# Performance work log

Measured on AMD Instinct MI355X. Metric: run time of the kernel, lower is better.

The kernel has to match this reference:

```python
import jax, jax.numpy as jnp
import numpy as np

N, T = 64, 256
TOTAL_NODES, C_IN = 25, 128          # c = 3200
NUM_SEEDS, C_OUT = 5, 3              # seeds flat dim = 15
NEW_NODES = 20
LIN_IN = TOTAL_NODES * C_IN + NUM_SEEDS * C_OUT  # 3215


def setup_inputs() -> dict:
    key = jax.random.key(0)
    k1, k2, k3 = jax.random.split(key, 3)
    x = jax.random.normal(k1, (N, T, TOTAL_NODES * C_IN), dtype=jnp.float32)
    seeds = jax.random.normal(k2, (N, T, NUM_SEEDS, C_OUT), dtype=jnp.float32)
    # Stacked weights of the `new_nodes` cloned Linear(LIN_IN, C_OUT) layers.
    W = jax.random.normal(k3, (NEW_NODES, C_OUT, LIN_IN), dtype=jnp.float32) * 0.02
    b = jnp.zeros((NEW_NODES, C_OUT), dtype=jnp.float32)
    return {"x": x, "seeds": seeds, "W": W, "b": b}


def reference(x, seeds, W, b):
    n, t, _ = x.shape
    mix = jnp.concatenate([x, seeds.reshape(n, t, -1)], axis=2)  # [n,t,LIN_IN]
    # Fuse all cloned small Linears into one batched GEMM, then layout as
    # torch.stack([...], dim=3): output [n, t, c_out, new_nodes].
    out = jnp.einsum('ntc,koc->ntok', mix, W) + b.T  # b.T: [c_out, new_nodes]
    return out
```

## Files before the change

### kernel.cpp

```cpp
#include <hip/hip_runtime.h>


#define NROWS    16384
#define CIN      3200
#define SEED_K   15
#define LIN_IN   3215
#define NCOL     60
#define KB_MAIN  100
#define KB_TOT   101
#define KB_CHUNK 25
#define WB_ELEMS (KB_TOT * 4 * 64 * 8)

typedef __attribute__((ext_vector_type(8))) __bf16 bf16x8;
typedef __attribute__((ext_vector_type(4))) float f32x4;
typedef __attribute__((ext_vector_type(8))) unsigned short ushort8;

__device__ unsigned short Wb_g[WB_ELEMS];

__device__ inline unsigned short f2bf_rne(float f) {
    unsigned int u = __builtin_bit_cast(unsigned int, f);
    u += 0x7fffu + ((u >> 16) & 1u);
    return (unsigned short)(u >> 16);
}

__device__ inline bf16x8 to_bf16x8(f32x4 a0, f32x4 a1) {
    ushort8 u;
    u[0] = f2bf_rne(a0[0]); u[1] = f2bf_rne(a0[1]);
    u[2] = f2bf_rne(a0[2]); u[3] = f2bf_rne(a0[3]);
    u[4] = f2bf_rne(a1[0]); u[5] = f2bf_rne(a1[1]);
    u[6] = f2bf_rne(a1[2]); u[7] = f2bf_rne(a1[3]);
    return __builtin_bit_cast(bf16x8, u);
}

__global__ void prep_B(const float* __restrict__ W) {
    int idx = blockIdx.x * blockDim.x + threadIdx.x;
    if (idx >= WB_ELEMS) return;
    int jj   = idx & 7;
    int lane = (idx >> 3) & 63;
    int nt   = (idx >> 9) & 3;
    int kb   = idx >> 11;
    int k = kb * 32 + (lane >> 4) * 8 + jj;
    int n = nt * 16 + (lane & 15);
    float v = 0.0f;
    if (k < LIN_IN && n < NCOL) {
        int o = n / 20, kn = n % 20;
        v = W[(kn * 3 + o) * LIN_IN + k];
    }
    Wb_g[idx] = f2bf_rne(v);
}

__global__ __launch_bounds__(256, 4) void gen_nodes_gemm(
    const float* __restrict__ x, const float* __restrict__ seeds,
    const float* __restrict__ b, float* __restrict__ out) {
    const int lane = threadIdx.x & 63;
    const int wave = threadIdx.x >> 6;
    const int quad = lane >> 4;
    const int l15  = lane & 15;
    const int row_base = blockIdx.x * 16;
    const int arow = row_base + l15;

    const float* xrow = x + (size_t)arow * CIN + quad * 8;

    f32x4 acc[4];
#pragma unroll
    for (int i = 0; i < 4; ++i) acc[i] = (f32x4){0.f, 0.f, 0.f, 0.f};

    const int kb0 = wave * KB_CHUNK;
    const int kb1 = kb0 + KB_CHUNK;

#pragma unroll 2
    for (int kb = kb0; kb < kb1; ++kb) {
        const f32x4* ap = (const f32x4*)(xrow + kb * 32);
        f32x4 a0 = ap[0];
        f32x4 a1 = ap[1];
        const unsigned short* bb = Wb_g + (size_t)kb * 2048 + lane * 8;
        bf16x8 b0 = *(const bf16x8*)(bb);
        bf16x8 b1 = *(const bf16x8*)(bb + 512);
        bf16x8 b2 = *(const bf16x8*)(bb + 1024);
        bf16x8 b3 = *(const bf16x8*)(bb + 1536);
        bf16x8 af = to_bf16x8(a0, a1);
        acc[0] = __builtin_amdgcn_mfma_f32_16x16x32_bf16(af, b0, acc[0], 0, 0, 0);
        acc[1] = __builtin_amdgcn_mfma_f32_16x16x32_bf16(af, b1, acc[1], 0, 0, 0);
        acc[2] = __builtin_amdgcn_mfma_f32_16x16x32_bf16(af, b2, acc[2], 0, 0, 0);
        acc[3] = __builtin_amdgcn_mfma_f32_16x16x32_bf16(af, b3, acc[3], 0, 0, 0);
    }

    if (wave == 3) {
        const float* srow = seeds + (size_t)arow * SEED_K;
        f32x4 s0 = {0.f, 0.f, 0.f, 0.f}, s1 = {0.f, 0.f, 0.f, 0.f};
#pragma unroll
        for (int j = 0; j < 4; ++j) {
            int c = quad * 8 + j;
            if (c < SEED_K) s0[j] = srow[c];
            if (c + 4 < SEED_K) s1[j] = srow[c + 4];
        }
        bf16x8 af = to_bf16x8(s0, s1);
        const unsigned short* bb = Wb_g + (size_t)KB_MAIN * 2048 + lane * 8;
        bf16x8 b0 = *(const bf16x8*)(bb);
        bf16x8 b1 = *(const bf16x8*)(bb + 512);
        bf16x8 b2 = *(const bf16x8*)(bb + 1024);
        bf16x8 b3 = *(const bf16x8*)(bb + 1536);
        acc[0] = __builtin_amdgcn_mfma_f32_16x16x32_bf16(af, b0, acc[0], 0, 0, 0);
        acc[1] = __builtin_amdgcn_mfma_f32_16x16x32_bf16(af, b1, acc[1], 0, 0, 0);
        acc[2] = __builtin_amdgcn_mfma_f32_16x16x32_bf16(af, b2, acc[2], 0, 0, 0);
        acc[3] = __builtin_amdgcn_mfma_f32_16x16x32_bf16(af, b3, acc[3], 0, 0, 0);
    }

    __shared__ float red[3][16][68];
    if (wave != 0) {
#pragma unroll
        for (int nt = 0; nt < 4; ++nt)
#pragma unroll
            for (int r = 0; r < 4; ++r)
                red[wave - 1][quad * 4 + r][nt * 16 + l15] = acc[nt][r];
    }
    __syncthreads();

    if (wave == 0) {
#pragma unroll
        for (int nt = 0; nt < 4; ++nt) {
            int j = nt * 16 + l15;
            if (j < NCOL) {
                float bias = b[(j % 20) * 3 + (j / 20)];
#pragma unroll
                for (int r = 0; r < 4; ++r) {
                    int m = quad * 4 + r;
                    float v = acc[nt][r] + red[0][m][j] + red[1][m][j]
                            + red[2][m][j] + bias;
                    out[(size_t)(row_base + m) * NCOL + j] = v;
                }
            }
        }
    }
}

extern "C" void kernel_launch(void* const* d_in, const int* in_sizes, int n_in,
                              void* d_out, int out_size, void* d_ws, size_t ws_size,
                              hipStream_t stream) {
    const float* x     = (const float*)d_in[0];
    const float* seeds = (const float*)d_in[1];
    const float* W     = (const float*)d_in[2];
    const float* b     = (const float*)d_in[3];
    float* out = (float*)d_out;
    (void)d_ws; (void)ws_size;

    prep_B<<<(WB_ELEMS + 255) / 256, 256, 0, stream>>>(W);
    gen_nodes_gemm<<<NROWS / 16, 256, 0, stream>>>(x, seeds, b, out);
}
```

Before: 306.8 us.

## Split K across two blocks per row group with prefetch and separate combine kernel

The GEMM is split so that each 16-row group is handled by two blocks, each covering half of K. Within each half the four waves interleave k-blocks with a stride of four, the next A tile is prefetched with nontemporal loads, and occupancy hints are raised. Partial sums go to a workspace and a new combine kernel adds the two halves plus a precomputed bias. The goal is more blocks in flight to hide the latency of the memory-bound x stream, at the cost of an extra kernel launch and a round trip of partials through memory.

```diff
diff --git a/kernel.cpp b/kernel.cpp
--- a/kernel.cpp
+++ b/kernel.cpp
@@ -8,14 +8,15 @@
 #define NCOL     60
 #define KB_MAIN  100
 #define KB_TOT   101
-#define KB_CHUNK 25
 #define WB_ELEMS (KB_TOT * 4 * 64 * 8)
+#define PART_N   (NROWS * NCOL)
 
 typedef __attribute__((ext_vector_type(8))) __bf16 bf16x8;
 typedef __attribute__((ext_vector_type(4))) float f32x4;
 typedef __attribute__((ext_vector_type(8))) unsigned short ushort8;
 
 __device__ unsigned short Wb_g[WB_ELEMS];
+__device__ __align__(16) float bias_g[64];
 
 __device__ inline unsigned short f2bf_rne(float f) {
     unsigned int u = __builtin_bit_cast(unsigned int, f);
@@ -32,9 +33,10 @@
     return __builtin_bit_cast(bf16x8, u);
 }
 
-__global__ void prep_B(const float* __restrict__ W) {
+__global__ void prep_B(const float* __restrict__ W, const float* __restrict__ b) {
     int idx = blockIdx.x * blockDim.x + threadIdx.x;
     if (idx >= WB_ELEMS) return;
+    if (idx < 64) bias_g[idx] = (idx < NCOL) ? b[(idx % 20) * 3 + (idx / 20)] : 0.f;
     int jj   = idx & 7;
     int lane = (idx >> 3) & 63;
     int nt   = (idx >> 9) & 3;
@@ -49,14 +51,16 @@
     Wb_g[idx] = f2bf_rne(v);
 }
 
-__global__ __launch_bounds__(256, 4) void gen_nodes_gemm(
+__global__ __launch_bounds__(256, 6) void gen_nodes_part(
     const float* __restrict__ x, const float* __restrict__ seeds,
-    const float* __restrict__ b, float* __restrict__ out) {
+    float* __restrict__ part) {
     const int lane = threadIdx.x & 63;
     const int wave = threadIdx.x >> 6;
     const int quad = lane >> 4;
     const int l15  = lane & 15;
-    const int row_base = blockIdx.x * 16;
+    const int rg   = blockIdx.x >> 1;
+    const int kh   = blockIdx.x & 1;
+    const int row_base = rg * 16;
     const int arow = row_base + l15;
 
     const float* xrow = x + (size_t)arow * CIN + quad * 8;
@@ -65,14 +69,20 @@
 #pragma unroll
     for (int i = 0; i < 4; ++i) acc[i] = (f32x4){0.f, 0.f, 0.f, 0.f};
 
-    const int kb0 = wave * KB_CHUNK;
-    const int kb1 = kb0 + KB_CHUNK;
+    const int kend = kh * 50 + 50;
+    int kb = kh * 50 + wave;
+    const f32x4* ap = (const f32x4*)(xrow + kb * 32);
+    f32x4 a0 = __builtin_nontemporal_load(ap);
+    f32x4 a1 = __builtin_nontemporal_load(ap + 1);
 
 #pragma unroll 2
-    for (int kb = kb0; kb < kb1; ++kb) {
-        const f32x4* ap = (const f32x4*)(xrow + kb * 32);
-        f32x4 a0 = ap[0];
-        f32x4 a1 = ap[1];
+    while (kb < kend) {
+        int kn = kb + 4;
+        int kc = (kn < KB_MAIN - 1) ? kn : (KB_MAIN - 1);
+        const f32x4* apn = (const f32x4*)(xrow + kc * 32);
+        f32x4 p0 = __builtin_nontemporal_load(apn);
+        f32x4 p1 = __builtin_nontemporal_load(apn + 1);
+
         const unsigned short* bb = Wb_g + (size_t)kb * 2048 + lane * 8;
         bf16x8 b0 = *(const bf16x8*)(bb);
         bf16x8 b1 = *(const bf16x8*)(bb + 512);
@@ -83,9 +93,11 @@
         acc[1] = __builtin_amdgcn_mfma_f32_16x16x32_bf16(af, b1, acc[1], 0, 0, 0);
         acc[2] = __builtin_amdgcn_mfma_f32_16x16x32_bf16(af, b2, acc[2], 0, 0, 0);
         acc[3] = __builtin_amdgcn_mfma_f32_16x16x32_bf16(af, b3, acc[3], 0, 0, 0);
+
+        a0 = p0; a1 = p1; kb = kn;
     }
 
-    if (wave == 3) {
+    if (kh == 1 && wave == 3) {
         const float* srow = seeds + (size_t)arow * SEED_K;
         f32x4 s0 = {0.f, 0.f, 0.f, 0.f}, s1 = {0.f, 0.f, 0.f, 0.f};
 #pragma unroll
@@ -117,21 +129,32 @@
     __syncthreads();
 
     if (wave == 0) {
+        float* pdst = part + (size_t)kh * PART_N;
 #pragma unroll
         for (int nt = 0; nt < 4; ++nt) {
             int j = nt * 16 + l15;
             if (j < NCOL) {
-                float bias = b[(j % 20) * 3 + (j / 20)];
 #pragma unroll
                 for (int r = 0; r < 4; ++r) {
                     int m = quad * 4 + r;
-                    float v = acc[nt][r] + red[0][m][j] + red[1][m][j]
-                            + red[2][m][j] + bias;
-                    out[(size_t)(row_base + m) * NCOL + j] = v;
+                    float v = acc[nt][r] + red[0][m][j] + red[1][m][j] + red[2][m][j];
+                    pdst[(size_t)(row_base + m) * NCOL + j] = v;
                 }
             }
         }
     }
+}
+
+__global__ __launch_bounds__(256) void combine(
+    const float* __restrict__ part, float* __restrict__ out) {
+    int idx = blockIdx.x * 256 + threadIdx.x;
+    int fl  = idx * 4;
+    f32x4 p0 = *(const f32x4*)(part + fl);
+    f32x4 p1 = *(const f32x4*)(part + PART_N + fl);
+    int jb = fl % NCOL;
+    f32x4 bv = *(const f32x4*)(bias_g + jb);
+    f32x4 o = p0 + p1 + bv;
+    *(f32x4*)(out + fl) = o;
 }
 
 extern "C" void kernel_launch(void* const* d_in, const int* in_sizes, int n_in,
@@ -141,9 +164,10 @@
     const float* seeds = (const float*)d_in[1];
     const float* W     = (const float*)d_in[2];
     const float* b     = (const float*)d_in[3];
-    float* out = (float*)d_out;
-    (void)d_ws; (void)ws_size;
+    float* out  = (float*)d_out;
+    float* part = (float*)d_ws;
 
-    prep_B<<<(WB_ELEMS + 255) / 256, 256, 0, stream>>>(W);
-    gen_nodes_gemm<<<NROWS / 16, 256, 0, stream>>>(x, seeds, b, out);
+    prep_B<<<(WB_ELEMS + 255) / 256, 256, 0, stream>>>(W, b);
+    gen_nodes_part<<<2048, 256, 0, stream>>>(x, seeds, part);
+    combine<<<PART_N / 4 / 256, 256, 0, stream>>>(part, out);
 }
```

New measurement: 310.6 us. About the same (+1.2%).
